# Kernel optimization log

Hardware: AMD Instinct MI355X
Metric: run time of the kernel (lower is better)

Reference implementation:

```python
import jax, jax.numpy as jnp
import numpy as np

THR = 0.5  # thresholds init arg


def _gcn_adj(exp, thr):
    """Dense normalized adjacency matching PyG GCNConv gcn_norm.
    exp: [dim, n_exp]. Graph has N = n_exp + 1 nodes (last node = token).
    Edges (src -> dst): (n_exp -> i) for every expert i, and (i -> j) for i < j
    when cosine_similarity(exp[:, i], exp[:, j]) > thr. Self-loops added, then
    symmetric normalization with in-degree: A_hat = D^-1/2 A D^-1/2.
    Returns A_hat with A_hat[dst, src] layout.
    """
    n_exp = exp.shape[1]
    N = n_exp + 1
    norms = jnp.maximum(jnp.linalg.norm(exp, axis=0), 1e-8)  # F.cosine_similarity eps
    en = exp / norms
    cos = en.T @ en  # [n_exp, n_exp]
    upper = jnp.triu(jnp.ones((n_exp, n_exp), dtype=bool), k=1)  # i < j
    e_mask = jnp.where(upper & (cos > thr), 1.0, 0.0).astype(exp.dtype)  # edge i->j
    A = jnp.zeros((N, N), dtype=exp.dtype)
    A = A.at[:n_exp, :n_exp].set(e_mask.T)   # A[dst=j, src=i]
    A = A.at[:n_exp, n_exp].set(1.0)          # token node -> each expert
    A = A + jnp.eye(N, dtype=exp.dtype)       # self loops
    deg = A.sum(axis=1)                        # in-degree (>= 1)
    d = jax.lax.rsqrt(deg)
    return A * d[:, None] * d[None, :]


def setup_inputs() -> dict:
    key = jax.random.key(0)
    ks = jax.random.split(key, 8)
    dim, n_exp, dg = 1024, 64, 256
    B, S = 2, 1024
    sc = lambda k, shape, fan: jax.random.normal(k, shape, jnp.float32) * (fan ** -0.5)
    return {
        "x": jax.random.normal(ks[0], (B, S, dim), jnp.float32),
        "X_param": jax.random.uniform(ks[1], (dim, n_exp), jnp.float32),  # torch.rand
        "mlp_w": sc(ks[2], (dim, dim), dim),
        "W0": sc(ks[3], (dim, dg), dim),
        "W1": sc(ks[4], (dg, dg), dg),
        "W2": sc(ks[5], (dg, dg), dg),
        "W3": sc(ks[6], (dg, dim), dg),
        "proj_w": sc(ks[7], (dim, 1), dim),
    }


def reference(x, X_param, mlp_w, W0, W1, W2, W3, proj_w):
    B, S, dim = x.shape
    n_exp = X_param.shape[1]
    xt = jax.nn.relu(x.reshape(-1, dim) @ mlp_w)      # [T, dim] tokens
    exp = jax.nn.relu(X_param.T @ mlp_w).T            # [dim, n_exp] experts (shared mlp)
    A = _gcn_adj(exp, THR)                            # [N, N], N = n_exp + 1
    T = xt.shape[0]
    # Layer 0 (dim -> dim_gcn): expert part of X W0 is shared across all tokens.
    expW = exp.T @ W0                                  # [n_exp, dg]
    h = jnp.concatenate(
        [jnp.broadcast_to(expW[None], (T,) + expW.shape), (xt @ W0)[:, None, :]],
        axis=1,
    )                                                  # [T, N, dg]
    h = jnp.einsum('nm,tmd->tnd', A, h)                # conv0 (no relu after it)
    # Middle layers: conv then relu
    h = jax.nn.relu(jnp.einsum('nm,tmd->tnd', A, h @ W1))
    h = jax.nn.relu(jnp.einsum('nm,tmd->tnd', A, h @ W2))
    # Last layer (dim_gcn -> dim), no relu
    h = jnp.einsum('nm,tmd->tnd', A, h @ W3)           # [T, N, dim]
    scores = (h @ proj_w)[..., 0][:, :n_exp]           # drop token node, [T, n_exp]
    out = jax.nn.softmax(scores, axis=-1)
    return out.reshape(B, S, n_exp)
```

## Files before the change

kernel.cpp:

```cpp
#include <hip/hip_runtime.h>
#include <hip/hip_bf16.h>
#include <math.h>

#define DIM 1024
#define NEXP 64
#define NN 65
#define DG 256
#define T_TOK 2048
#define THR_EDGE 0.5f

typedef __attribute__((ext_vector_type(8))) short bf16x8;
typedef __attribute__((ext_vector_type(4))) float f32x4;
typedef unsigned short ushort_t;
typedef __attribute__((ext_vector_type(8))) unsigned short us8;

static __device__ __forceinline__ ushort_t f2bf(float x) {
  unsigned u = __float_as_uint(x);
  unsigned r = (u + 0x7FFFu + ((u >> 16) & 1u)) >> 16;
  return (ushort_t)r;
}
static __device__ __forceinline__ float bf2f(ushort_t h) {
  return __uint_as_float(((unsigned)h) << 16);
}


__global__ __launch_bounds__(256) void k_expT_ks(const float* __restrict__ Xp,
                                                 const float* __restrict__ mlp,
                                                 float* __restrict__ part) {
  int i0 = blockIdx.y * 4;
  int j = blockIdx.x * 256 + threadIdx.x;
  int k0 = blockIdx.z * 128;
  float acc0 = 0.f, acc1 = 0.f, acc2 = 0.f, acc3 = 0.f;
#pragma unroll 4
  for (int k = k0; k < k0 + 128; ++k) {
    float m = mlp[(size_t)k * DIM + j];
    const float* xr = &Xp[(size_t)k * NEXP + i0];
    acc0 = fmaf(xr[0], m, acc0);
    acc1 = fmaf(xr[1], m, acc1);
    acc2 = fmaf(xr[2], m, acc2);
    acc3 = fmaf(xr[3], m, acc3);
  }
  size_t base = ((size_t)blockIdx.z * NEXP + i0) * DIM + j;
  part[base + 0 * DIM] = acc0;
  part[base + 1 * DIM] = acc1;
  part[base + 2 * DIM] = acc2;
  part[base + 3 * DIM] = acc3;
}

__global__ __launch_bounds__(256) void k_expT_red(const float* __restrict__ part,
                                                  float* __restrict__ expT,
                                                  float* __restrict__ expTT) {
  int e = blockIdx.x * 256 + threadIdx.x;
  int i = e >> 10, j = e & 1023;
  float v = 0.f;
#pragma unroll
  for (int kc = 0; kc < 8; ++kc)
    v += part[(size_t)kc * (NEXP * DIM) + e];
  v = fmaxf(v, 0.f);
  expT[e] = v;
  expTT[(size_t)j * NEXP + i] = v;
}

__global__ __launch_bounds__(256) void k_W01(const float* __restrict__ W0,
                                             const float* __restrict__ W1,
                                             ushort_t* __restrict__ Bh,
                                             ushort_t* __restrict__ Bl) {
  int i = blockIdx.x;
  int d = threadIdx.x;
  float acc = 0.f;
#pragma unroll 4
  for (int k = 0; k < DG; ++k)
    acc = fmaf(W0[i * DG + k], W1[k * DG + d], acc);
  int dt = d >> 4, c = d & 15, ks = i >> 5, kg = (i >> 3) & 3, j = i & 7;
  size_t idx = (((size_t)dt * 32 + ks) * 64 + kg * 16 + c) * 8 + j;
  ushort_t h = f2bf(acc);
  Bh[idx] = h;
  Bl[idx] = f2bf(acc - bf2f(h));
}

__global__ __launch_bounds__(256) void k_w3p(const float* __restrict__ W3,
                                             const float* __restrict__ pw,
                                             float* __restrict__ w3p) {
  __shared__ float red[4];
  int i = blockIdx.x;
  int tid = threadIdx.x, lane = tid & 63, w = tid >> 6;
  const float* r = &W3[(size_t)i * DIM];
  float s = r[tid] * pw[tid]
          + r[tid + 256] * pw[tid + 256]
          + r[tid + 512] * pw[tid + 512]
          + r[tid + 768] * pw[tid + 768];
#pragma unroll
  for (int off = 32; off > 0; off >>= 1)
    s += __shfl_down(s, off, 64);
  if (lane == 0) red[w] = s;
  __syncthreads();
  if (tid == 0) w3p[i] = red[0] + red[1] + red[2] + red[3];
}

__global__ __launch_bounds__(256) void k_splitX(const float* __restrict__ X,
                                                ushort_t* __restrict__ Xh,
                                                ushort_t* __restrict__ Xl) {
  size_t base = ((size_t)blockIdx.x * 256 + threadIdx.x) * 8;
  us8 h, l;
#pragma unroll
  for (int u = 0; u < 8; ++u) {
    float v = X[base + u];
    ushort_t hh = f2bf(v);
    h[u] = hh;
    l[u] = f2bf(v - bf2f(hh));
  }
  *(us8*)(Xh + base) = h;
  *(us8*)(Xl + base) = l;
}

__global__ __launch_bounds__(256) void k_splitB(const float* __restrict__ B,
                                                ushort_t* __restrict__ Bh,
                                                ushort_t* __restrict__ Bl,
                                                int K, int N) {
  int k0 = blockIdx.x * 8;
  int d = blockIdx.y * 256 + threadIdx.x;
  int KS = K >> 5;
  int dt = d >> 4, c = d & 15, ks = k0 >> 5, kg = (k0 >> 3) & 3;
  size_t idx = (((size_t)dt * KS + ks) * 64 + kg * 16 + c) * 8;
  us8 h, l;
#pragma unroll
  for (int j = 0; j < 8; ++j) {
    float v = B[(size_t)(k0 + j) * N + d];
    ushort_t hh = f2bf(v);
    h[j] = hh;
    l[j] = f2bf(v - bf2f(hh));
  }
  *(us8*)(Bh + idx) = h;
  *(us8*)(Bl + idx) = l;
}

__global__ __launch_bounds__(256) void k_cos(const float* __restrict__ expTT,
                                             float* __restrict__ D) {
  __shared__ float part[4][NEXP];
  int i = blockIdx.x;
  int tid = threadIdx.x;
  int j = tid & 63, qd = tid >> 6;
  float acc = 0.f;
  int d0 = qd * 256;
  for (int d = d0; d < d0 + 256; ++d) {
    float ei = expTT[(size_t)d * NEXP + i];
    float ej = expTT[(size_t)d * NEXP + j];
    acc = fmaf(ei, ej, acc);
  }
  part[qd][j] = acc;
  __syncthreads();
  if (tid < NEXP)
    D[i * NEXP + tid] = part[0][tid] + part[1][tid] + part[2][tid] + part[3][tid];
}

__global__ __launch_bounds__(256) void k_splitW2(const float* __restrict__ W2,
                                                 ushort_t* __restrict__ Wh,
                                                 ushort_t* __restrict__ Wl) {
  int k = blockIdx.x;
  int d = threadIdx.x;
  float w = W2[(size_t)k * DG + d];
  ushort_t h = f2bf(w);
  ushort_t l = f2bf(w - bf2f(h));
  int dt = d >> 4, c = d & 15, ks = k >> 5, kg = (k >> 3) & 3, j = k & 7;
  int idx = (((dt * 8 + ks) * 64) + kg * 16 + c) * 8 + j;
  Wh[idx] = h;
  Wl[idx] = l;
}

__global__ __launch_bounds__(256) void k_buildA(const float* __restrict__ D,
                                                float* __restrict__ Ahat,
                                                float* __restrict__ q) {
  __shared__ float nrm[NEXP];
  __shared__ float Ar[NN][NN];
  __shared__ float Al[NN][NN];
  __shared__ float dd[NN];
  __shared__ float a0[NN];
  int tid = threadIdx.x;
  if (tid < NEXP) nrm[tid] = fmaxf(sqrtf(D[tid * NEXP + tid]), 1e-8f);
  __syncthreads();
  for (int e = tid; e < NN * NN; e += 256) {
    int n = e / NN, m = e - n * NN;
    float v = 0.f;
    if (n == m) v = 1.f;
    else if (m == NEXP) v = (n < NEXP) ? 1.f : 0.f;
    else if (n < NEXP && m < n) {
      float c = D[m * NEXP + n] / (nrm[m] * nrm[n]);
      v = (c > THR_EDGE) ? 1.f : 0.f;
    }
    Ar[n][m] = v;
  }
  __syncthreads();
  if (tid < NN) {
    float s = 0.f;
    for (int m = 0; m < NN; ++m) s += Ar[tid][m];
    dd[tid] = 1.0f / sqrtf(s);
  }
  __syncthreads();
  for (int e = tid; e < NN * NN; e += 256) {
    int n = e / NN, m = e - n * NN;
    float v = Ar[n][m] * dd[n] * dd[m];
    Al[n][m] = v;
    Ahat[e] = v;
  }
  __syncthreads();
  if (tid < NN) a0[tid] = Al[tid][NEXP];
  __syncthreads();
  if (tid < NN) {
    float s = 0.f;
    for (int m = 0; m < NN; ++m) s = fmaf(Al[tid][m], a0[m], s);
    q[tid] = s;
  }
}

__global__ __launch_bounds__(256) void k_expW(const float* __restrict__ expT,
                                              const float* __restrict__ W0,
                                              float* __restrict__ expW) {
  int m = blockIdx.x, d = threadIdx.x;
  float acc = 0.f;
#pragma unroll 4
  for (int k = 0; k < DIM; ++k)
    acc = fmaf(expT[m * DIM + k], W0[k * DG + d], acc);
  expW[m * DG + d] = acc;
}

__global__ __launch_bounds__(256) void k_CW1(const float* __restrict__ Ahat,
                                             const float* __restrict__ expW,
                                             const float* __restrict__ W1,
                                             float* __restrict__ CW1) {
  __shared__ float c0[DG];
  int n = blockIdx.x, d = threadIdx.x;
  float acc = 0.f;
  for (int m = 0; m < NEXP; ++m)
    acc = fmaf(Ahat[n * NN + m], expW[m * DG + d], acc);
  c0[d] = acc;
  __syncthreads();
  float b = 0.f;
#pragma unroll 4
  for (int k = 0; k < DG; ++k)
    b = fmaf(c0[k], W1[k * DG + d], b);
  CW1[n * DG + d] = b;
}

__global__ __launch_bounds__(256) void k_P(const float* __restrict__ Ahat,
                                           const float* __restrict__ CW1,
                                           float* __restrict__ P) {
  int n = blockIdx.x, d = threadIdx.x;
  float acc = 0.f;
  for (int m = 0; m < NN; ++m)
    acc = fmaf(Ahat[n * NN + m], CW1[m * DG + d], acc);
  P[n * DG + d] = acc;
}

template <int NT, bool RELU, bool OSPLIT>
__global__ __launch_bounds__(256) void k_mgemm(const ushort_t* __restrict__ Ah,
                                               const ushort_t* __restrict__ Al,
                                               const ushort_t* __restrict__ Bh,
                                               const ushort_t* __restrict__ Bl,
                                               float* __restrict__ C,
                                               ushort_t* __restrict__ Ch,
                                               ushort_t* __restrict__ Cl,
                                               int M, int N, int K) {
  int tid = threadIdx.x, lane = tid & 63, w = tid >> 6;
  int t0 = blockIdx.x * 64 + w * 16;
  int n0 = blockIdx.y * (NT * 16);
  int row = lane & 15, kg = lane >> 4;
  int KS = K >> 5;

  f32x4 acc[NT];
#pragma unroll
  for (int nt = 0; nt < NT; ++nt) acc[nt] = (f32x4){0.f, 0.f, 0.f, 0.f};

  const ushort_t* pA0 = Ah + (size_t)(t0 + row) * K + kg * 8;
  const ushort_t* pA1 = Al + (size_t)(t0 + row) * K + kg * 8;

  for (int kc = 0; kc < KS; kc += 8) {
    bf16x8 ah[8], al[8];
#pragma unroll
    for (int ks = 0; ks < 8; ++ks) {
      ah[ks] = *(const bf16x8*)(pA0 + (kc + ks) * 32);
      al[ks] = *(const bf16x8*)(pA1 + (kc + ks) * 32);
    }
#pragma unroll
    for (int nt = 0; nt < NT; ++nt) {
      int dt = (n0 >> 4) + nt;
      const ushort_t* pBh = Bh + ((size_t)dt * KS + kc) * 512 + lane * 8;
      const ushort_t* pBl = Bl + ((size_t)dt * KS + kc) * 512 + lane * 8;
      bf16x8 bh[8], bl[8];
#pragma unroll
      for (int ks = 0; ks < 8; ++ks) {
        bh[ks] = *(const bf16x8*)(pBh + ks * 512);
        bl[ks] = *(const bf16x8*)(pBl + ks * 512);
      }
#pragma unroll
      for (int ks = 0; ks < 8; ++ks) {
        acc[nt] = __builtin_amdgcn_mfma_f32_16x16x32_bf16(ah[ks], bh[ks], acc[nt], 0, 0, 0);
        acc[nt] = __builtin_amdgcn_mfma_f32_16x16x32_bf16(al[ks], bh[ks], acc[nt], 0, 0, 0);
        acc[nt] = __builtin_amdgcn_mfma_f32_16x16x32_bf16(ah[ks], bl[ks], acc[nt], 0, 0, 0);
        acc[nt] = __builtin_amdgcn_mfma_f32_16x16x32_bf16(al[ks], bl[ks], acc[nt], 0, 0, 0);
      }
    }
  }

#pragma unroll
  for (int nt = 0; nt < NT; ++nt) {
    int cc = n0 + nt * 16 + row;
#pragma unroll
    for (int r = 0; r < 4; ++r) {
      float v = acc[nt][r];
      if (RELU) v = fmaxf(v, 0.f);
      size_t o = (size_t)(t0 + kg * 4 + r) * N + cc;
      if (OSPLIT) {
        ushort_t h = f2bf(v);
        Ch[o] = h;
        Cl[o] = f2bf(v - bf2f(h));
      } else {
        C[o] = v;
      }
    }
  }
}

__global__ __launch_bounds__(256) void k_mix(const float* __restrict__ V,
                                             const float* __restrict__ P,
                                             const float* __restrict__ Ahat,
                                             const float* __restrict__ q,
                                             ushort_t* __restrict__ Gh,
                                             ushort_t* __restrict__ Gl,
                                             int n0, int nch) {
  int t = blockIdx.x;
  int k = threadIdx.x;
  float v = V[(size_t)t * DG + k];
  float r[NN];
#pragma unroll
  for (int m = 0; m < NN; ++m)
    r[m] = fmaxf(fmaf(q[m], v, P[m * DG + k]), 0.f);
  for (int nn = 0; nn < nch; ++nn) {
    const float* arow = &Ahat[(size_t)(n0 + nn) * NN];
    float a0 = 0.f, a1 = 0.f, a2 = 0.f, a3 = 0.f;
#pragma unroll
    for (int m = 0; m < 16; ++m) {
      a0 = fmaf(arow[m +  0], r[m +  0], a0);
      a1 = fmaf(arow[m + 16], r[m + 16], a1);
      a2 = fmaf(arow[m + 32], r[m + 32], a2);
      a3 = fmaf(arow[m + 48], r[m + 48], a3);
    }
    float acc = ((a0 + a1) + (a2 + a3)) + arow[64] * r[64];
    size_t idx = ((size_t)nn * T_TOK + t) * DG + k;
    ushort_t h = f2bf(acc);
    Gh[idx] = h;
    Gl[idx] = f2bf(acc - bf2f(h));
  }
}

__global__ __launch_bounds__(256, 2) void k_zgemm(const ushort_t* __restrict__ Gh,
                                                  const ushort_t* __restrict__ Gl,
                                                  const ushort_t* __restrict__ Wh,
                                                  const ushort_t* __restrict__ Wl,
                                                  const float* __restrict__ w3p,
                                                  float* __restrict__ s2T,
                                                  int n0) {
  int tid = threadIdx.x, lane = tid & 63, w = tid >> 6;
  int ny = blockIdx.y;
  int t0 = blockIdx.x * 64 + w * 16;
  int row = lane & 15, kg = lane >> 4;

  const ushort_t* Ah = Gh + ((size_t)ny * T_TOK + t0 + row) * DG + kg * 8;
  const ushort_t* Al = Gl + ((size_t)ny * T_TOK + t0 + row) * DG + kg * 8;
  bf16x8 ah[8], al[8];
#pragma unroll
  for (int ks = 0; ks < 8; ++ks) {
    ah[ks] = *(const bf16x8*)(Ah + ks * 32);
    al[ks] = *(const bf16x8*)(Al + ks * 32);
  }

  f32x4 acc[16];
#pragma unroll
  for (int dt = 0; dt < 16; ++dt) acc[dt] = (f32x4){0.f, 0.f, 0.f, 0.f};

#pragma unroll
  for (int dt = 0; dt < 16; ++dt) {
    const ushort_t* Bh = Wh + (size_t)dt * 4096 + lane * 8;
    const ushort_t* Bl = Wl + (size_t)dt * 4096 + lane * 8;
    bf16x8 bh[8], bl[8];
#pragma unroll
    for (int ks = 0; ks < 8; ++ks) {
      bh[ks] = *(const bf16x8*)(Bh + ks * 512);
      bl[ks] = *(const bf16x8*)(Bl + ks * 512);
    }
#pragma unroll
    for (int ks = 0; ks < 8; ++ks) {
      acc[dt] = __builtin_amdgcn_mfma_f32_16x16x32_bf16(ah[ks], bh[ks], acc[dt], 0, 0, 0);
      acc[dt] = __builtin_amdgcn_mfma_f32_16x16x32_bf16(al[ks], bh[ks], acc[dt], 0, 0, 0);
      acc[dt] = __builtin_amdgcn_mfma_f32_16x16x32_bf16(ah[ks], bl[ks], acc[dt], 0, 0, 0);
      acc[dt] = __builtin_amdgcn_mfma_f32_16x16x32_bf16(al[ks], bl[ks], acc[dt], 0, 0, 0);
    }
  }

  float v0 = 0.f, v1 = 0.f, v2 = 0.f, v3 = 0.f;
#pragma unroll
  for (int dt = 0; dt < 16; ++dt) {
    float wpd = w3p[dt * 16 + row];
    v0 = fmaf(fmaxf(acc[dt][0], 0.f), wpd, v0);
    v1 = fmaf(fmaxf(acc[dt][1], 0.f), wpd, v1);
    v2 = fmaf(fmaxf(acc[dt][2], 0.f), wpd, v2);
    v3 = fmaf(fmaxf(acc[dt][3], 0.f), wpd, v3);
  }
#pragma unroll
  for (int off = 1; off < 16; off <<= 1) {
    v0 += __shfl_xor(v0, off, 64);
    v1 += __shfl_xor(v1, off, 64);
    v2 += __shfl_xor(v2, off, 64);
    v3 += __shfl_xor(v3, off, 64);
  }
  if (row == 0) {
    int t = t0 + kg * 4;
    int n = n0 + ny;
    s2T[(size_t)(t + 0) * NN + n] = v0;
    s2T[(size_t)(t + 1) * NN + n] = v1;
    s2T[(size_t)(t + 2) * NN + n] = v2;
    s2T[(size_t)(t + 3) * NN + n] = v3;
  }
}

__global__ __launch_bounds__(64) void k_final(const float* __restrict__ s2T,
                                              const float* __restrict__ Ahat,
                                              float* __restrict__ out) {
  __shared__ float s2l[NN];
  int t = blockIdx.x;
  int j = threadIdx.x;
  s2l[j] = s2T[(size_t)t * NN + j];
  if (j == 0) s2l[NEXP] = s2T[(size_t)t * NN + NEXP];
  __syncthreads();
  float sc = 0.f;
  for (int m = 0; m < NN; ++m)
    sc = fmaf(Ahat[j * NN + m], s2l[m], sc);
  float mx = sc;
#pragma unroll
  for (int off = 32; off > 0; off >>= 1)
    mx = fmaxf(mx, __shfl_xor(mx, off, 64));
  float e = expf(sc - mx);
  float sum = e;
#pragma unroll
  for (int off = 32; off > 0; off >>= 1)
    sum += __shfl_xor(sum, off, 64);
  out[(size_t)t * NEXP + j] = e / sum;
}

extern "C" void kernel_launch(void* const* d_in, const int* in_sizes, int n_in,
                              void* d_out, int out_size, void* d_ws, size_t ws_size,
                              hipStream_t stream) {
  (void)in_sizes; (void)n_in; (void)out_size; (void)ws_size;
  const float* x   = (const float*)d_in[0];
  const float* Xp  = (const float*)d_in[1];
  const float* mlp = (const float*)d_in[2];
  const float* W0  = (const float*)d_in[3];
  const float* W1  = (const float*)d_in[4];
  const float* W2  = (const float*)d_in[5];
  const float* W3  = (const float*)d_in[6];
  const float* pw  = (const float*)d_in[7];
  float* out = (float*)d_out;
  float* ws = (float*)d_ws;

  float* expT  = ws + 0;
  float* expTT = ws + 65536;
  float* w3p   = ws + 131072;
  float* D     = ws + 131328;
  float* Ahat  = ws + 135424;
  float* q     = ws + 139664;
  float* expW  = ws + 139744;
  float* CW1   = ws + 156128;
  float* P     = ws + 172768;
  float* s2T   = ws + 189408;
  float* V     = ws + 322528;
  float* part  = ws + 846816;
  ushort_t* W01f_h = (ushort_t*)(ws + 1371104);
  ushort_t* W01f_l = (ushort_t*)(ws + 1502176);
  float* arena = ws + 1633248;
  ushort_t* Xh    = (ushort_t*)(arena);
  ushort_t* Xl    = (ushort_t*)(arena + 1048576);
  ushort_t* mlpf_h = (ushort_t*)(arena + 2097152);
  ushort_t* mlpf_l = (ushort_t*)(arena + 2621440);
  ushort_t* XTh   = (ushort_t*)(arena + 3145728);
  ushort_t* XTl   = (ushort_t*)(arena + 4194304);
  ushort_t* Gc_h  = (ushort_t*)(arena);
  ushort_t* Gc_l  = (ushort_t*)(arena + 8650752);
  ushort_t* W2f_h = (ushort_t*)(ws + 65536);
  ushort_t* W2f_l = (ushort_t*)(ws + 65536 + 32768);

  k_expT_ks<<<dim3(4, 16, 8), dim3(256), 0, stream>>>(Xp, mlp, part);
  k_expT_red<<<dim3(256), dim3(256), 0, stream>>>(part, expT, expTT);
  k_W01<<<dim3(1024), dim3(256), 0, stream>>>(W0, W1, W01f_h, W01f_l);
  k_w3p<<<dim3(256), dim3(256), 0, stream>>>(W3, pw, w3p);
  k_splitX<<<dim3(1024), dim3(256), 0, stream>>>(x, Xh, Xl);
  k_splitB<<<dim3(128, 4), dim3(256), 0, stream>>>(mlp, mlpf_h, mlpf_l, DIM, DIM);
  k_cos<<<dim3(64), dim3(256), 0, stream>>>(expTT, D);
  k_splitW2<<<dim3(256), dim3(256), 0, stream>>>(W2, W2f_h, W2f_l);
  k_buildA<<<dim3(1), dim3(256), 0, stream>>>(D, Ahat, q);
  k_expW<<<dim3(64), dim3(256), 0, stream>>>(expT, W0, expW);
  k_CW1<<<dim3(65), dim3(256), 0, stream>>>(Ahat, expW, W1, CW1);
  k_P<<<dim3(65), dim3(256), 0, stream>>>(Ahat, CW1, P);
  k_mgemm<4, true, true><<<dim3(32, 16), dim3(256), 0, stream>>>(
      Xh, Xl, mlpf_h, mlpf_l, nullptr, XTh, XTl, T_TOK, DIM, DIM);
  k_mgemm<2, false, false><<<dim3(32, 8), dim3(256), 0, stream>>>(
      XTh, XTl, W01f_h, W01f_l, V, nullptr, nullptr, T_TOK, DG, DIM);
  k_mix<<<dim3(T_TOK), dim3(256), 0, stream>>>(V, P, Ahat, q, Gc_h, Gc_l, 0, 33);
  k_zgemm<<<dim3(32, 33), dim3(256), 0, stream>>>(Gc_h, Gc_l, W2f_h, W2f_l, w3p, s2T, 0);
  k_mix<<<dim3(T_TOK), dim3(256), 0, stream>>>(V, P, Ahat, q, Gc_h, Gc_l, 33, 32);
  k_zgemm<<<dim3(32, 32), dim3(256), 0, stream>>>(Gc_h, Gc_l, W2f_h, W2f_l, w3p, s2T, 33);
  k_final<<<dim3(T_TOK), dim3(64), 0, stream>>>(s2T, Ahat, out);
}
```

Measured before the change: 591.9 us.

## Split zgemm output columns across grid z with partial sums reduced in final

The z-GEMM now splits its 16 output column tiles into 4 groups along a new grid z dimension. Each block computes only 4 tiles, which cuts accumulator registers and lets launch bounds allow 4 blocks per CU instead of 2. Each group writes a partial projected score into its own slice of a new workspace buffer, and the final kernel sums the 4 partials before the adjacency mix and softmax. The cost is that each block reloads and re-converts the same A operand (Gh/Gl) 4 times, plus a larger partial-score buffer and extra reads in the final kernel.

Measured after the change: 545.0 us. 1.09x faster.

```diff
diff --git a/kernel.cpp b/kernel.cpp
--- a/kernel.cpp
+++ b/kernel.cpp
@@ -352,15 +352,16 @@
   }
 }
 
-__global__ __launch_bounds__(256, 2) void k_zgemm(const ushort_t* __restrict__ Gh,
+__global__ __launch_bounds__(256, 4) void k_zgemm(const ushort_t* __restrict__ Gh,
                                                   const ushort_t* __restrict__ Gl,
                                                   const ushort_t* __restrict__ Wh,
                                                   const ushort_t* __restrict__ Wl,
                                                   const float* __restrict__ w3p,
-                                                  float* __restrict__ s2T,
+                                                  float* __restrict__ s2p,
                                                   int n0) {
   int tid = threadIdx.x, lane = tid & 63, w = tid >> 6;
   int ny = blockIdx.y;
+  int dtg = blockIdx.z;
   int t0 = blockIdx.x * 64 + w * 16;
   int row = lane & 15, kg = lane >> 4;
 
@@ -373,37 +374,35 @@
     al[ks] = *(const bf16x8*)(Al + ks * 32);
   }
 
-  f32x4 acc[16];
-#pragma unroll
-  for (int dt = 0; dt < 16; ++dt) acc[dt] = (f32x4){0.f, 0.f, 0.f, 0.f};
-
-#pragma unroll
-  for (int dt = 0; dt < 16; ++dt) {
+  f32x4 acc[4];
+#pragma unroll
+  for (int nt = 0; nt < 4; ++nt) acc[nt] = (f32x4){0.f, 0.f, 0.f, 0.f};
+
+#pragma unroll
+  for (int nt = 0; nt < 4; ++nt) {
+    int dt = dtg * 4 + nt;
     const ushort_t* Bh = Wh + (size_t)dt * 4096 + lane * 8;
     const ushort_t* Bl = Wl + (size_t)dt * 4096 + lane * 8;
-    bf16x8 bh[8], bl[8];
 #pragma unroll
     for (int ks = 0; ks < 8; ++ks) {
-      bh[ks] = *(const bf16x8*)(Bh + ks * 512);
-      bl[ks] = *(const bf16x8*)(Bl + ks * 512);
-    }
-#pragma unroll
-    for (int ks = 0; ks < 8; ++ks) {
-      acc[dt] = __builtin_amdgcn_mfma_f32_16x16x32_bf16(ah[ks], bh[ks], acc[dt], 0, 0, 0);
-      acc[dt] = __builtin_amdgcn_mfma_f32_16x16x32_bf16(al[ks], bh[ks], acc[dt], 0, 0, 0);
-      acc[dt] = __builtin_amdgcn_mfma_f32_16x16x32_bf16(ah[ks], bl[ks], acc[dt], 0, 0, 0);
-      acc[dt] = __builtin_amdgcn_mfma_f32_16x16x32_bf16(al[ks], bl[ks], acc[dt], 0, 0, 0);
+      bf16x8 bh = *(const bf16x8*)(Bh + ks * 512);
+      bf16x8 bl = *(const bf16x8*)(Bl + ks * 512);
+      acc[nt] = __builtin_amdgcn_mfma_f32_16x16x32_bf16(ah[ks], bh, acc[nt], 0, 0, 0);
+      acc[nt] = __builtin_amdgcn_mfma_f32_16x16x32_bf16(al[ks], bh, acc[nt], 0, 0, 0);
+      acc[nt] = __builtin_amdgcn_mfma_f32_16x16x32_bf16(ah[ks], bl, acc[nt], 0, 0, 0);
+      acc[nt] = __builtin_amdgcn_mfma_f32_16x16x32_bf16(al[ks], bl, acc[nt], 0, 0, 0);
     }
   }
 
   float v0 = 0.f, v1 = 0.f, v2 = 0.f, v3 = 0.f;
 #pragma unroll
-  for (int dt = 0; dt < 16; ++dt) {
+  for (int nt = 0; nt < 4; ++nt) {
+    int dt = dtg * 4 + nt;
     float wpd = w3p[dt * 16 + row];
-    v0 = fmaf(fmaxf(acc[dt][0], 0.f), wpd, v0);
-    v1 = fmaf(fmaxf(acc[dt][1], 0.f), wpd, v1);
-    v2 = fmaf(fmaxf(acc[dt][2], 0.f), wpd, v2);
-    v3 = fmaf(fmaxf(acc[dt][3], 0.f), wpd, v3);
+    v0 = fmaf(fmaxf(acc[nt][0], 0.f), wpd, v0);
+    v1 = fmaf(fmaxf(acc[nt][1], 0.f), wpd, v1);
+    v2 = fmaf(fmaxf(acc[nt][2], 0.f), wpd, v2);
+    v3 = fmaf(fmaxf(acc[nt][3], 0.f), wpd, v3);
   }
 #pragma unroll
   for (int off = 1; off < 16; off <<= 1) {
@@ -415,21 +414,34 @@
   if (row == 0) {
     int t = t0 + kg * 4;
     int n = n0 + ny;
-    s2T[(size_t)(t + 0) * NN + n] = v0;
-    s2T[(size_t)(t + 1) * NN + n] = v1;
-    s2T[(size_t)(t + 2) * NN + n] = v2;
-    s2T[(size_t)(t + 3) * NN + n] = v3;
-  }
-}
-
-__global__ __launch_bounds__(64) void k_final(const float* __restrict__ s2T,
+    size_t b = (size_t)dtg * T_TOK;
+    s2p[(b + t + 0) * NN + n] = v0;
+    s2p[(b + t + 1) * NN + n] = v1;
+    s2p[(b + t + 2) * NN + n] = v2;
+    s2p[(b + t + 3) * NN + n] = v3;
+  }
+}
+
+__global__ __launch_bounds__(64) void k_final(const float* __restrict__ s2p,
                                               const float* __restrict__ Ahat,
                                               float* __restrict__ out) {
   __shared__ float s2l[NN];
   int t = blockIdx.x;
   int j = threadIdx.x;
-  s2l[j] = s2T[(size_t)t * NN + j];
-  if (j == 0) s2l[NEXP] = s2T[(size_t)t * NN + NEXP];
+  {
+    float s = 0.f;
+#pragma unroll
+    for (int g = 0; g < 4; ++g)
+      s += s2p[((size_t)g * T_TOK + t) * NN + j];
+    s2l[j] = s;
+    if (j == 0) {
+      float s64 = 0.f;
+#pragma unroll
+      for (int g = 0; g < 4; ++g)
+        s64 += s2p[((size_t)g * T_TOK + t) * NN + NEXP];
+      s2l[NEXP] = s64;
+    }
+  }
   __syncthreads();
   float sc = 0.f;
   for (int m = 0; m < NN; ++m)
@@ -484,8 +496,10 @@
   ushort_t* XTl   = (ushort_t*)(arena + 4194304);
   ushort_t* Gc_h  = (ushort_t*)(arena);
   ushort_t* Gc_l  = (ushort_t*)(arena + 8650752);
+  float* s2p = ws + 18934752;
   ushort_t* W2f_h = (ushort_t*)(ws + 65536);
   ushort_t* W2f_l = (ushort_t*)(ws + 65536 + 32768);
+  (void)s2T;
 
   k_expT_ks<<<dim3(4, 16, 8), dim3(256), 0, stream>>>(Xp, mlp, part);
   k_expT_red<<<dim3(256), dim3(256), 0, stream>>>(part, expT, expTT);
@@ -504,8 +518,8 @@
   k_mgemm<2, false, false><<<dim3(32, 8), dim3(256), 0, stream>>>(
       XTh, XTl, W01f_h, W01f_l, V, nullptr, nullptr, T_TOK, DG, DIM);
   k_mix<<<dim3(T_TOK), dim3(256), 0, stream>>>(V, P, Ahat, q, Gc_h, Gc_l, 0, 33);
-  k_zgemm<<<dim3(32, 33), dim3(256), 0, stream>>>(Gc_h, Gc_l, W2f_h, W2f_l, w3p, s2T, 0);
+  k_zgemm<<<dim3(32, 33, 4), dim3(256), 0, stream>>>(Gc_h, Gc_l, W2f_h, W2f_l, w3p, s2p, 0);
   k_mix<<<dim3(T_TOK), dim3(256), 0, stream>>>(V, P, Ahat, q, Gc_h, Gc_l, 33, 32);
-  k_zgemm<<<dim3(32, 32), dim3(256), 0, stream>>>(Gc_h, Gc_l, W2f_h, W2f_l, w3p, s2T, 33);
-  k_final<<<dim3(T_TOK), dim3(64), 0, stream>>>(s2T, Ahat, out);
-}
+  k_zgemm<<<dim3(32, 32, 4), dim3(256), 0, stream>>>(Gc_h, Gc_l, W2f_h, W2f_l, w3p, s2p, 33);
+  k_final<<<dim3(T_TOK), dim3(64), 0, stream>>>(s2p, Ahat, out);
+}
```
